# Optimization experiments

Hardware: AMD Instinct MI355X
Metric: run time of the kernel (lower is better)

## Reference

```python
import jax, jax.numpy as jnp
import numpy as np

DISTANCE_THRESHOLD = 100.0  # squared-distance threshold (cdist**2 <= thresh)
NO_CODE_ID = -1


def setup_inputs() -> dict:
    key = jax.random.key(0)
    kx, kc = jax.random.split(key)
    x = jax.random.normal(kx, (2, 1024, 64), dtype=jnp.float32)      # [b, s, d] query tokens
    codes = jax.random.normal(kc, (50000, 64), dtype=jnp.float32)    # [n, d] active code bank
    return {"x": x, "codes": codes}


def reference(x, codes):
    # squared euclidean distances, matching torch.cdist(x, codes) ** 2
    x2 = jnp.sum(x * x, axis=-1, keepdims=True)            # [b, s, 1]
    c2 = jnp.sum(codes * codes, axis=-1)                   # [n]
    cross = jnp.einsum('bsd,nd->bsn', x, codes)            # [b, s, n]
    d2 = jnp.maximum(x2 + c2 - 2.0 * cross, 0.0)           # clamp tiny negatives, cdist >= 0

    within = jnp.any(d2 <= DISTANCE_THRESHOLD, axis=-1)    # [b, s]
    nn_ids = jnp.argmin(d2, axis=-1)                       # [b, s]
    return jnp.where(within, nn_ids, NO_CODE_ID)
```

## Files before the change

### kernel.cpp

```cpp
#include <hip/hip_runtime.h>

#define NTOK   2048
#define DIM    64
#define NCODES 50000
#define THRESH 100.0f
#define BIG    3.0e38f
#define MARGIN 4.0f
#define NBLK   391
#define BM32   1564
#define BM32P  1568
#define NCG    56

typedef __attribute__((ext_vector_type(8)))  __bf16 bf16x8;
typedef __attribute__((ext_vector_type(16))) float  float16;

__device__ __forceinline__ unsigned short f2bf(float f) {
    union { float f; unsigned int u; } v; v.f = f;
    unsigned int r = v.u + 0x7FFF + ((v.u >> 16) & 1);
    return (unsigned short)(r >> 16);
}
__device__ __forceinline__ unsigned int pack2(float a, float b) {
    return (unsigned int)f2bf(a) | ((unsigned int)f2bf(b) << 16);
}

__global__ __launch_bounds__(256)
void nn_prep_kernel(const float* __restrict__ x, const float* __restrict__ codes,
                    unsigned short* __restrict__ cbf, unsigned short* __restrict__ xbf,
                    float* __restrict__ c2, float* __restrict__ x2,
                    float* __restrict__ bm32) {
    int g = blockIdx.x * 256 + threadIdx.x;
    if (g < NTOK * 4) {
        int t = g >> 2;
        bm32[(size_t)t * BM32P + BM32 + (g & 3)] = BIG;
    }
    int row = g >> 2;
    int seg = g & 3;
    const float* src;
    unsigned short* dst;
    float* nrm;
    if (row < NCODES) {
        src = codes + (size_t)row * DIM + seg * 16;
        dst = cbf + (size_t)row * DIM + seg * 16;
        nrm = (seg == 0) ? (c2 + row) : nullptr;
    } else if (row < NCODES + NTOK) {
        int r = row - NCODES;
        src = x + (size_t)r * DIM + seg * 16;
        dst = xbf + (size_t)r * DIM + seg * 16;
        nrm = (seg == 0) ? (x2 + r) : nullptr;
    } else {
        return;
    }
    float4 v0 = ((const float4*)src)[0];
    float4 v1 = ((const float4*)src)[1];
    float4 v2 = ((const float4*)src)[2];
    float4 v3 = ((const float4*)src)[3];
    float s = 0.f;
    s = fmaf(v0.x, v0.x, s); s = fmaf(v0.y, v0.y, s);
    s = fmaf(v0.z, v0.z, s); s = fmaf(v0.w, v0.w, s);
    s = fmaf(v1.x, v1.x, s); s = fmaf(v1.y, v1.y, s);
    s = fmaf(v1.z, v1.z, s); s = fmaf(v1.w, v1.w, s);
    s = fmaf(v2.x, v2.x, s); s = fmaf(v2.y, v2.y, s);
    s = fmaf(v2.z, v2.z, s); s = fmaf(v2.w, v2.w, s);
    s = fmaf(v3.x, v3.x, s); s = fmaf(v3.y, v3.y, s);
    s = fmaf(v3.z, v3.z, s); s = fmaf(v3.w, v3.w, s);
    uint4 lo, hi;
    lo.x = pack2(v0.x, v0.y); lo.y = pack2(v0.z, v0.w);
    lo.z = pack2(v1.x, v1.y); lo.w = pack2(v1.z, v1.w);
    hi.x = pack2(v2.x, v2.y); hi.y = pack2(v2.z, v2.w);
    hi.z = pack2(v3.x, v3.y); hi.w = pack2(v3.z, v3.w);
    *(uint4*)dst = lo;
    *(uint4*)(dst + 8) = hi;
    s += __shfl_xor(s, 1);
    s += __shfl_xor(s, 2);
    if (nrm) *nrm = s;
}

__global__ __launch_bounds__(256, 2)
void nn_stageA_kernel(const unsigned short* __restrict__ xbf,
                      const unsigned short* __restrict__ cbf,
                      const float* __restrict__ c2g,
                      float* __restrict__ bm32) {
    __shared__ __bf16 cs[128 * 72];
    __shared__ float  c2s[128];

    const int tid  = threadIdx.x;
    const int w    = tid >> 6;
    const int lane = tid & 63;
    const int l31  = lane & 31;
    const int h    = lane >> 5;
    const int g0   = blockIdx.x * 7;
    const int nb   = min(7, NBLK - g0);
    const int t0   = blockIdx.y * 256;

    bf16x8 bfr[4][2];
#pragma unroll
    for (int s = 0; s < 4; ++s)
#pragma unroll
        for (int nj = 0; nj < 2; ++nj)
            bfr[s][nj] = *(const bf16x8*)&xbf[
                (size_t)(t0 + w * 64 + nj * 32 + l31) * DIM + s * 16 + h * 8];

    uint4 pr[4];
    float prc;
    auto prefetch = [&](int blk) {
        int n0 = blk * 128;
#pragma unroll
        for (int it = 0; it < 4; ++it) {
            int g = it * 256 + tid;
            int row = g >> 3, seg = g & 7;
            int n = n0 + row;
            pr[it] = (n < NCODES) ? *(const uint4*)(cbf + (size_t)n * DIM + seg * 8)
                                  : make_uint4(0, 0, 0, 0);
        }
        if (tid < 128) {
            int n = n0 + tid;
            prc = (n < NCODES) ? c2g[n] : BIG;
        }
    };
    prefetch(g0);

    for (int t = 0; t < nb; ++t) {
        const int blk = g0 + t;
        __syncthreads();

#pragma unroll
        for (int it = 0; it < 4; ++it) {
            int g = it * 256 + tid;
            int row = g >> 3, seg = g & 7;
            *(uint4*)&cs[row * 72 + seg * 8] = pr[it];
        }
        if (tid < 128) c2s[tid] = prc;
        if (t + 1 < nb) prefetch(blk + 1);
        __syncthreads();

        float16 acc[4][2];
#pragma unroll
        for (int mi = 0; mi < 4; ++mi) {
#pragma unroll
            for (int g2 = 0; g2 < 4; ++g2) {
                float4 c4 = *(float4*)&c2s[mi * 32 + g2 * 8 + 4 * h];
#pragma unroll
                for (int i = 0; i < 4; ++i) {
                    float iv = -0.5f * ((float*)&c4)[i];
                    acc[mi][0][g2 * 4 + i] = iv;
                    acc[mi][1][g2 * 4 + i] = iv;
                }
            }
        }

#pragma unroll
        for (int s = 0; s < 4; ++s) {
            bf16x8 a[4];
#pragma unroll
            for (int mi = 0; mi < 4; ++mi)
                a[mi] = *(bf16x8*)&cs[(mi * 32 + l31) * 72 + s * 16 + h * 8];
#pragma unroll
            for (int mi = 0; mi < 4; ++mi)
#pragma unroll
                for (int nj = 0; nj < 2; ++nj)
                    acc[mi][nj] = __builtin_amdgcn_mfma_f32_32x32x16_bf16(
                        a[mi], bfr[s][nj], acc[mi][nj], 0, 0, 0);
        }

#pragma unroll
        for (int nj = 0; nj < 2; ++nj) {
#pragma unroll
            for (int mi = 0; mi < 4; ++mi) {
                float m = acc[mi][nj][0];
#pragma unroll
                for (int r = 1; r < 16; ++r) m = fmaxf(m, acc[mi][nj][r]);
                m = fmaxf(m, __shfl_xor(m, 32));
                if (lane < 32) {
                    int token = t0 + w * 64 + nj * 32 + lane;
                    bm32[(size_t)token * BM32P + blk * 4 + mi] = -2.0f * m;
                }
            }
        }
    }
}

__global__ __launch_bounds__(256)
void nn_finalize_kernel(const float* __restrict__ x,
                        const float* __restrict__ codes,
                        const float* __restrict__ c2,
                        const float* __restrict__ x2,
                        const float* __restrict__ bm32,
                        int* __restrict__ out) {
    __shared__ float redf[8];
    __shared__ int   redi[4];
    __shared__ int   queue[BM32P];
    __shared__ int   qcount;
    __shared__ float gshare;

    const int tid  = threadIdx.x;
    const int w    = tid >> 6;
    const int lane = tid & 63;
    const int t    = blockIdx.x;
    const float* bm = bm32 + (size_t)t * BM32P;

    if (tid == 0) qcount = 0;

    float v[7];
    float g = BIG;
#pragma unroll
    for (int k = 0; k < 7; ++k) {
        int b = tid + k * 256;
        v[k] = (b < BM32P) ? bm[b] : BIG;
        g = fminf(g, v[k]);
    }
#pragma unroll
    for (int m = 1; m < 64; m <<= 1) g = fminf(g, __shfl_xor(g, m));
    if (lane == 0) redf[w] = g;
    __syncthreads();
    if (tid == 0)
        gshare = fminf(fminf(redf[0], redf[1]), fminf(redf[2], redf[3])) + MARGIN;
    __syncthreads();
    const float th = gshare;

#pragma unroll
    for (int k = 0; k < 7; ++k) {
        int b = tid + k * 256;
        if (b < BM32P && v[k] <= th) {
            int slot = atomicAdd(&qcount, 1);
            queue[slot] = b;
        }
    }
    __syncthreads();
    const int nq = qcount;

    const int half = lane & 1;
    float4 xh[8];
#pragma unroll
    for (int q = 0; q < 8; ++q)
        xh[q] = *(const float4*)(x + (size_t)t * DIM + half * 32 + q * 4);
    const float x2v = x2[t];

    float bv = BIG;
    int   bi = 0x7fffffff;
    for (int e = w; e < nq; e += 4) {
        int blk = queue[e];
        int n = blk * 32 + (lane >> 1);
        if (n < NCODES) {
            const float4* cp = (const float4*)(codes + (size_t)n * DIM + half * 32);
            float d = 0.f;
#pragma unroll
            for (int q = 0; q < 8; ++q) {
                float4 c4 = cp[q];
                d = fmaf(xh[q].x, c4.x, d);
                d = fmaf(xh[q].y, c4.y, d);
                d = fmaf(xh[q].z, c4.z, d);
                d = fmaf(xh[q].w, c4.w, d);
            }
            d += __shfl_xor(d, 1);
            float d2 = fmaxf(fmaf(-2.f, d, x2v + c2[n]), 0.f);
            if (d2 < bv || (d2 == bv && n < bi)) { bv = d2; bi = n; }
        }
    }
#pragma unroll
    for (int m = 1; m < 64; m <<= 1) {
        float vv = __shfl_xor(bv, m);
        int   ii = __shfl_xor(bi, m);
        if (vv < bv || (vv == bv && ii < bi)) { bv = vv; bi = ii; }
    }
    if (lane == 0) { redf[4 + w] = bv; redi[w] = bi; }
    __syncthreads();
    if (tid == 0) {
        float fb = BIG;
        int   fi = 0x7fffffff;
#pragma unroll
        for (int i = 0; i < 4; ++i) {
            float vv = redf[4 + i];
            int   ii = redi[i];
            if (vv < fb || (vv == fb && ii < fi)) { fb = vv; fi = ii; }
        }
        out[t] = (fb <= THRESH) ? fi : -1;
    }
}

extern "C" void kernel_launch(void* const* d_in, const int* in_sizes, int n_in,
                              void* d_out, int out_size, void* d_ws, size_t ws_size,
                              hipStream_t stream) {
    const float* x     = (const float*)d_in[0];
    const float* codes = (const float*)d_in[1];

    float* c2 = (float*)d_ws;
    float* x2 = c2 + 50048;
    unsigned short* cbf = (unsigned short*)(x2 + NTOK);
    unsigned short* xbf = cbf + (size_t)NCODES * DIM;
    float* bm32 = (float*)(xbf + (size_t)NTOK * DIM);
    int* out = (int*)d_out;

    nn_prep_kernel<<<814, 256, 0, stream>>>(x, codes, cbf, xbf, c2, x2, bm32);
    nn_stageA_kernel<<<dim3(NCG, 8), 256, 0, stream>>>(xbf, cbf, c2, bm32);
    nn_finalize_kernel<<<NTOK, 256, 0, stream>>>(x, codes, c2, x2, bm32, out);
}
```

Baseline: 113.2 us.

## Fuse code bf16 conversion and norms into stage A, recompute norms in finalize

The prep kernel no longer converts the 50000-entry code bank to bf16 or computes code norms; it only handles the 2048 query tokens. Stage A now loads fp32 codes directly, computes the squared norms and bf16 packing in its prefetch, and fills shared memory. Finalize recomputes each candidate code's norm from the fp32 values it already loads. Stage A's grid grows to 64 column groups with an uneven 7/6 block split to balance the 391 blocks. This removes a full write and re-read of the bf16 code bank and the c2 array, at the cost of doubling global reads in stage A (fp32 instead of bf16) across the 8 token tiles, plus extra ALU work.

```diff
diff --git a/kernel.cpp b/kernel.cpp
--- a/kernel.cpp
+++ b/kernel.cpp
@@ -9,7 +9,7 @@
 #define NBLK   391
 #define BM32   1564
 #define BM32P  1568
-#define NCG    56
+#define NCG    64
 
 typedef __attribute__((ext_vector_type(8)))  __bf16 bf16x8;
 typedef __attribute__((ext_vector_type(16))) float  float16;
@@ -24,32 +24,19 @@
 }
 
 __global__ __launch_bounds__(256)
-void nn_prep_kernel(const float* __restrict__ x, const float* __restrict__ codes,
-                    unsigned short* __restrict__ cbf, unsigned short* __restrict__ xbf,
-                    float* __restrict__ c2, float* __restrict__ x2,
+void nn_prep_kernel(const float* __restrict__ x,
+                    unsigned short* __restrict__ xbf,
+                    float* __restrict__ x2,
                     float* __restrict__ bm32) {
     int g = blockIdx.x * 256 + threadIdx.x;
-    if (g < NTOK * 4) {
+    {
         int t = g >> 2;
         bm32[(size_t)t * BM32P + BM32 + (g & 3)] = BIG;
     }
     int row = g >> 2;
     int seg = g & 3;
-    const float* src;
-    unsigned short* dst;
-    float* nrm;
-    if (row < NCODES) {
-        src = codes + (size_t)row * DIM + seg * 16;
-        dst = cbf + (size_t)row * DIM + seg * 16;
-        nrm = (seg == 0) ? (c2 + row) : nullptr;
-    } else if (row < NCODES + NTOK) {
-        int r = row - NCODES;
-        src = x + (size_t)r * DIM + seg * 16;
-        dst = xbf + (size_t)r * DIM + seg * 16;
-        nrm = (seg == 0) ? (x2 + r) : nullptr;
-    } else {
-        return;
-    }
+    const float* src = x + (size_t)row * DIM + seg * 16;
+    unsigned short* dst = xbf + (size_t)row * DIM + seg * 16;
     float4 v0 = ((const float4*)src)[0];
     float4 v1 = ((const float4*)src)[1];
     float4 v2 = ((const float4*)src)[2];
@@ -72,13 +59,12 @@
     *(uint4*)(dst + 8) = hi;
     s += __shfl_xor(s, 1);
     s += __shfl_xor(s, 2);
-    if (nrm) *nrm = s;
+    if (seg == 0) x2[row] = s;
 }
 
 __global__ __launch_bounds__(256, 2)
 void nn_stageA_kernel(const unsigned short* __restrict__ xbf,
-                      const unsigned short* __restrict__ cbf,
-                      const float* __restrict__ c2g,
+                      const float* __restrict__ codes,
                       float* __restrict__ bm32) {
     __shared__ __bf16 cs[128 * 72];
     __shared__ float  c2s[128];
@@ -88,8 +74,9 @@
     const int lane = tid & 63;
     const int l31  = lane & 31;
     const int h    = lane >> 5;
-    const int g0   = blockIdx.x * 7;
-    const int nb   = min(7, NBLK - g0);
+    const int gi   = blockIdx.x;
+    const int g0   = 6 * gi + min(gi, 7);
+    const int nb   = (gi < 7) ? 7 : 6;
     const int t0   = blockIdx.y * 256;
 
     bf16x8 bfr[4][2];
@@ -100,21 +87,38 @@
             bfr[s][nj] = *(const bf16x8*)&xbf[
                 (size_t)(t0 + w * 64 + nj * 32 + l31) * DIM + s * 16 + h * 8];
 
-    uint4 pr[4];
-    float prc;
+    uint4 pr[2][2];
+    float prc[2];
     auto prefetch = [&](int blk) {
         int n0 = blk * 128;
 #pragma unroll
-        for (int it = 0; it < 4; ++it) {
-            int g = it * 256 + tid;
-            int row = g >> 3, seg = g & 7;
+        for (int it = 0; it < 2; ++it) {
+            int slot = it * 256 + tid;
+            int row = slot >> 2, seg = slot & 3;
             int n = n0 + row;
-            pr[it] = (n < NCODES) ? *(const uint4*)(cbf + (size_t)n * DIM + seg * 8)
-                                  : make_uint4(0, 0, 0, 0);
-        }
-        if (tid < 128) {
-            int n = n0 + tid;
-            prc = (n < NCODES) ? c2g[n] : BIG;
+            float4 f0, f1, f2, f3;
+            if (n < NCODES) {
+                const float4* p = (const float4*)(codes + (size_t)n * DIM + seg * 16);
+                f0 = p[0]; f1 = p[1]; f2 = p[2]; f3 = p[3];
+            } else {
+                f0 = f1 = f2 = f3 = make_float4(0.f, 0.f, 0.f, 0.f);
+            }
+            float s = 0.f;
+            s = fmaf(f0.x, f0.x, s); s = fmaf(f0.y, f0.y, s);
+            s = fmaf(f0.z, f0.z, s); s = fmaf(f0.w, f0.w, s);
+            s = fmaf(f1.x, f1.x, s); s = fmaf(f1.y, f1.y, s);
+            s = fmaf(f1.z, f1.z, s); s = fmaf(f1.w, f1.w, s);
+            s = fmaf(f2.x, f2.x, s); s = fmaf(f2.y, f2.y, s);
+            s = fmaf(f2.z, f2.z, s); s = fmaf(f2.w, f2.w, s);
+            s = fmaf(f3.x, f3.x, s); s = fmaf(f3.y, f3.y, s);
+            s = fmaf(f3.z, f3.z, s); s = fmaf(f3.w, f3.w, s);
+            pr[it][0].x = pack2(f0.x, f0.y); pr[it][0].y = pack2(f0.z, f0.w);
+            pr[it][0].z = pack2(f1.x, f1.y); pr[it][0].w = pack2(f1.z, f1.w);
+            pr[it][1].x = pack2(f2.x, f2.y); pr[it][1].y = pack2(f2.z, f2.w);
+            pr[it][1].z = pack2(f3.x, f3.y); pr[it][1].w = pack2(f3.z, f3.w);
+            s += __shfl_xor(s, 1);
+            s += __shfl_xor(s, 2);
+            prc[it] = (n < NCODES) ? s : BIG;
         }
     };
     prefetch(g0);
@@ -124,12 +128,13 @@
         __syncthreads();
 
 #pragma unroll
-        for (int it = 0; it < 4; ++it) {
-            int g = it * 256 + tid;
-            int row = g >> 3, seg = g & 7;
-            *(uint4*)&cs[row * 72 + seg * 8] = pr[it];
-        }
-        if (tid < 128) c2s[tid] = prc;
+        for (int it = 0; it < 2; ++it) {
+            int slot = it * 256 + tid;
+            int row = slot >> 2, seg = slot & 3;
+            *(uint4*)&cs[row * 72 + seg * 16] = pr[it][0];
+            *(uint4*)&cs[row * 72 + seg * 16 + 8] = pr[it][1];
+            if (seg == 0) c2s[row] = prc[it];
+        }
         if (t + 1 < nb) prefetch(blk + 1);
         __syncthreads();
 
@@ -182,7 +187,6 @@
 __global__ __launch_bounds__(256)
 void nn_finalize_kernel(const float* __restrict__ x,
                         const float* __restrict__ codes,
-                        const float* __restrict__ c2,
                         const float* __restrict__ x2,
                         const float* __restrict__ bm32,
                         int* __restrict__ out) {
@@ -242,17 +246,33 @@
         int n = blk * 32 + (lane >> 1);
         if (n < NCODES) {
             const float4* cp = (const float4*)(codes + (size_t)n * DIM + half * 32);
+            float4 c4[8];
+#pragma unroll
+            for (int q = 0; q < 8; ++q) c4[q] = cp[q];
             float d = 0.f;
 #pragma unroll
             for (int q = 0; q < 8; ++q) {
-                float4 c4 = cp[q];
-                d = fmaf(xh[q].x, c4.x, d);
-                d = fmaf(xh[q].y, c4.y, d);
-                d = fmaf(xh[q].z, c4.z, d);
-                d = fmaf(xh[q].w, c4.w, d);
+                d = fmaf(xh[q].x, c4[q].x, d);
+                d = fmaf(xh[q].y, c4[q].y, d);
+                d = fmaf(xh[q].z, c4[q].z, d);
+                d = fmaf(xh[q].w, c4[q].w, d);
             }
             d += __shfl_xor(d, 1);
-            float d2 = fmaxf(fmaf(-2.f, d, x2v + c2[n]), 0.f);
+            float sa = 0.f, sb = 0.f;
+#pragma unroll
+            for (int q = 0; q < 4; ++q) {
+                sa = fmaf(c4[q].x, c4[q].x, sa); sa = fmaf(c4[q].y, c4[q].y, sa);
+                sa = fmaf(c4[q].z, c4[q].z, sa); sa = fmaf(c4[q].w, c4[q].w, sa);
+            }
+#pragma unroll
+            for (int q = 4; q < 8; ++q) {
+                sb = fmaf(c4[q].x, c4[q].x, sb); sb = fmaf(c4[q].y, c4[q].y, sb);
+                sb = fmaf(c4[q].z, c4[q].z, sb); sb = fmaf(c4[q].w, c4[q].w, sb);
+            }
+            float mysum = sa + sb;
+            float other = __shfl_xor(mysum, 1);
+            float c2v = half ? (other + mysum) : (mysum + other);
+            float d2 = fmaxf(fmaf(-2.f, d, x2v + c2v), 0.f);
             if (d2 < bv || (d2 == bv && n < bi)) { bv = d2; bi = n; }
         }
     }
@@ -283,14 +303,12 @@
     const float* x     = (const float*)d_in[0];
     const float* codes = (const float*)d_in[1];
 
-    float* c2 = (float*)d_ws;
-    float* x2 = c2 + 50048;
-    unsigned short* cbf = (unsigned short*)(x2 + NTOK);
-    unsigned short* xbf = cbf + (size_t)NCODES * DIM;
+    float* x2 = (float*)d_ws;
+    unsigned short* xbf = (unsigned short*)(x2 + NTOK);
     float* bm32 = (float*)(xbf + (size_t)NTOK * DIM);
     int* out = (int*)d_out;
 
-    nn_prep_kernel<<<814, 256, 0, stream>>>(x, codes, cbf, xbf, c2, x2, bm32);
-    nn_stageA_kernel<<<dim3(NCG, 8), 256, 0, stream>>>(xbf, cbf, c2, bm32);
-    nn_finalize_kernel<<<NTOK, 256, 0, stream>>>(x, codes, c2, x2, bm32, out);
-}
+    nn_prep_kernel<<<32, 256, 0, stream>>>(x, xbf, x2, bm32);
+    nn_stageA_kernel<<<dim3(NCG, 8), 256, 0, stream>>>(xbf, codes, bm32);
+    nn_finalize_kernel<<<NTOK, 256, 0, stream>>>(x, codes, x2, bm32, out);
+}
```

Result: no change. 112.8 us (-0.3%).
